# Optimization experiments

Hardware: AMD Instinct MI355X
Metric: run time of the kernel (lower is better)

Reference implementation:

```python
import jax, jax.numpy as jnp
import numpy as np

N_NODES = 100000
N_EDGES = 1600000
F_IN = 64
F_HID = 64


def setup_inputs() -> dict:
    key = jax.random.key(0)
    k = jax.random.split(key, 6)
    x = jax.random.normal(k[0], (N_NODES, F_IN), dtype=jnp.float32)
    edge_src = jax.random.randint(k[1], (N_EDGES,), 0, N_NODES, dtype=jnp.int32)
    edge_dst = jax.random.randint(k[2], (N_EDGES,), 0, N_NODES, dtype=jnp.int32)
    W1 = jax.random.normal(k[3], (2 * F_IN, F_HID), dtype=jnp.float32) * 0.05
    b1 = jnp.zeros((F_HID,), dtype=jnp.float32)
    W2 = jax.random.normal(k[4], (2 * F_HID, F_HID), dtype=jnp.float32) * 0.05
    b2 = jnp.zeros((F_HID,), dtype=jnp.float32)
    return {"x": x, "edge_src": edge_src, "edge_dst": edge_dst,
            "W1": W1, "b1": b1, "W2": W2, "b2": b2}


def _mean_aggregate(x, edge_src, edge_dst):
    # gather neighbor features along edges, segment-mean into destination nodes
    msgs = x[edge_src]                                            # [E, F]
    summed = jax.ops.segment_sum(msgs, edge_dst, num_segments=N_NODES)  # [N, F]
    cnt = jax.ops.segment_sum(jnp.ones_like(edge_dst, dtype=x.dtype),
                              edge_dst, num_segments=N_NODES)      # [N]
    # nodes with no neighbors -> zero vector (matches torch loop behavior)
    return summed / jnp.maximum(cnt, 1.0)[:, None]


def _sage_layer(x, edge_src, edge_dst, W, b):
    neigh_mean = _mean_aggregate(x, edge_src, edge_dst)
    h = jnp.concatenate([x, neigh_mean], axis=1)                  # [N, 2F]
    return jax.nn.relu(h @ W + b)


def reference(x, edge_src, edge_dst, W1, b1, W2, b2):
    h = _sage_layer(x, edge_src, edge_dst, W1, b1)
    h = _sage_layer(h, edge_src, edge_dst, W2, b2)
    return h
```

## Files before the change

kernel.cpp:

```cpp
#include <hip/hip_runtime.h>
#include <hip/hip_bf16.h>


constexpr int N_NODES = 100000;
constexpr int N_EDGES = 1600000;
constexpr int F = 64;
constexpr int SH = 9;
constexpr int SPAN = 1 << SH;
constexpr int NBK = 256;
constexpr int NBK_USED = (N_NODES + SPAN - 1) / SPAN;
constexpr int PART_T = 512;
constexpr int PART_E = 4096;
constexpr int PART_BLOCKS = (N_EDGES + PART_E - 1) / PART_E;
constexpr int COUNT_BLOCKS = (N_EDGES + 2047) / 2048;
constexpr int LDW = 136;

typedef short short8 __attribute__((ext_vector_type(8)));
typedef float floatx4 __attribute__((ext_vector_type(4)));

__device__ __forceinline__ float bf2f(ushort u) {
    union { unsigned int i; float f; } c; c.i = (unsigned int)u << 16; return c.f;
}
__device__ __forceinline__ ushort f2bf(float v) {
    union { float f; unsigned int i; } c; c.f = v;
    unsigned int r = c.i + 0x7fffu + ((c.i >> 16) & 1u);
    return (ushort)(r >> 16);
}


__global__ void __launch_bounds__(256)
count_kernel(const int* __restrict__ edst, int* __restrict__ bcnt) {
    __shared__ int lb[NBK];
    int t = threadIdx.x;
    lb[t] = 0;
    __syncthreads();
    int base = blockIdx.x * 2048;
    #pragma unroll
    for (int k = 0; k < 8; ++k) {
        int e = base + k * 256 + t;
        if (e < N_EDGES) atomicAdd(&lb[edst[e] >> SH], 1);
    }
    __syncthreads();
    if (lb[t]) atomicAdd(&bcnt[t], lb[t]);
}

__global__ void __launch_bounds__(512)
scan_prep_kernel(const int* __restrict__ bcnt, int* __restrict__ bbase,
                 int* __restrict__ bcur, int* __restrict__ rp,
                 const float* __restrict__ W1, const float* __restrict__ W2,
                 ushort* __restrict__ Wt1, ushort* __restrict__ Wt2) {
    __shared__ int sb[NBK];
    int t = threadIdx.x;
    if (t < NBK) sb[t] = bcnt[t];
    __syncthreads();
    if (t == 0) {
        int run = 0;
        for (int i = 0; i < NBK; ++i) { int v = sb[i]; sb[i] = run; run += v; }
        rp[N_NODES] = run;
    }
    __syncthreads();
    if (t < NBK) { bbase[t] = sb[t]; bcur[t] = sb[t]; }
    for (int i = t; i < 2 * F * F; i += 512) {
        int k = i >> 6, f = i & 63;
        Wt1[f * LDW + k] = f2bf(W1[i]);
        Wt2[f * LDW + k] = f2bf(W2[i]);
    }
}

__global__ void __launch_bounds__(PART_T)
part_kernel(const int* __restrict__ esrc, const int* __restrict__ edst,
            int* __restrict__ bcur, int2* __restrict__ ebuf) {
    __shared__ int cnt[NBK];
    __shared__ int lbase[NBK];
    __shared__ int gbase[NBK];
    __shared__ int2 stage[PART_E];
    int t = threadIdx.x;
    if (t < NBK) cnt[t] = 0;
    __syncthreads();
    int base = blockIdx.x * PART_E;
    int2 ed[8]; int bk[8]; int rk[8];
    #pragma unroll
    for (int k = 0; k < 8; ++k) {
        int e = base + k * PART_T + t;
        if (e < N_EDGES) {
            ed[k].x = esrc[e];
            ed[k].y = edst[e];
            bk[k] = ed[k].y >> SH;
            rk[k] = atomicAdd(&cnt[bk[k]], 1);
        } else {
            bk[k] = -1; rk[k] = 0; ed[k] = make_int2(0, 0);
        }
    }
    __syncthreads();
    {
        int v = 0;
        if (t < NBK) { v = cnt[t]; lbase[t] = v; }
        __syncthreads();
        for (int off = 1; off < NBK; off <<= 1) {
            int add = 0;
            if (t < NBK && t >= off) add = lbase[t - off];
            __syncthreads();
            if (t < NBK) lbase[t] += add;
            __syncthreads();
        }
        if (t < NBK) lbase[t] -= v;
    }
    __syncthreads();
    if (t < NBK) gbase[t] = cnt[t] ? atomicAdd(&bcur[t], cnt[t]) : 0;
    __syncthreads();
    #pragma unroll
    for (int k = 0; k < 8; ++k)
        if (bk[k] >= 0) stage[lbase[bk[k]] + rk[k]] = ed[k];
    __syncthreads();
    {
        int w = t >> 6, lane = t & 63;
        for (int b = w * 32; b < w * 32 + 32; ++b) {
            int len = cnt[b], l0 = lbase[b], g0 = gbase[b];
            for (int i = lane; i < len; i += 64) ebuf[g0 + i] = stage[l0 + i];
        }
    }
}

__global__ void __launch_bounds__(512)
csr_bucket_kernel(const int2* __restrict__ ebuf, const int* __restrict__ bbase,
                  const int* __restrict__ bcnt,
                  int* __restrict__ rp, int* __restrict__ ss) {
    __shared__ int sdeg[SPAN];
    __shared__ int sc[SPAN];
    int b = blockIdx.x;
    int lo = b << SH;
    int bstart = bbase[b];
    int bn = bcnt[b];
    int t = threadIdx.x;

    sdeg[t] = 0;
    __syncthreads();
    for (int i = t; i < bn; i += 512)
        atomicAdd(&sdeg[ebuf[bstart + i].y - lo], 1);
    __syncthreads();

    int a = sdeg[t];
    sc[t] = a;
    __syncthreads();
    for (int off = 1; off < SPAN; off <<= 1) {
        int v = sc[t];
        int add = (t >= off) ? sc[t - off] : 0;
        __syncthreads();
        sc[t] = v + add;
        __syncthreads();
    }
    int ex = sc[t] - a;
    sdeg[t] = ex;
    if (lo + t < N_NODES) rp[lo + t] = bstart + ex;
    __syncthreads();

    for (int i = t; i < bn; i += 512) {
        int2 p = ebuf[bstart + i];
        int pos = atomicAdd(&sdeg[p.y - lo], 1);
        ss[bstart + pos] = p.x;
    }
}

__global__ void __launch_bounds__(256)
conv_kernel(const float* __restrict__ x, ushort* __restrict__ xh) {
    int i = blockIdx.x * 256 + threadIdx.x;
    float4 v = ((const float4*)x)[i];
    ushort4 o;
    o.x = f2bf(v.x); o.y = f2bf(v.y); o.z = f2bf(v.z); o.w = f2bf(v.w);
    ((ushort4*)xh)[i] = o;
}

__global__ void __launch_bounds__(512)
fused_sage_kernel(const ushort* __restrict__ xh,
                  const int* __restrict__ rp,
                  const int* __restrict__ ss,
                  const ushort* __restrict__ Wt,
                  const float* __restrict__ bias,
                  ushort* __restrict__ out_bf,
                  float* __restrict__ out_f)
{
    __shared__ ushort sWt[F * LDW];
    __shared__ ushort cin[32 * LDW];

    {
        const int* src = (const int*)Wt;
        int* dst = (int*)sWt;
        for (int i = threadIdx.x; i < F * LDW / 2; i += 512) dst[i] = src[i];
    }

    const int w    = threadIdx.x >> 6;
    const int lane = threadIdx.x & 63;
    const int half = lane >> 5;
    const int p    = lane & 31;

    const unsigned int* __restrict__ xw = (const unsigned int*)xh;

    for (int q = 0; q < 4; ++q) {
        const int n = blockIdx.x * 32 + w * 4 + q;
        int start = rp[n];
        int end   = rp[n + 1];
        float ax = 0.0f, ay = 0.0f;

        int i = start;
        for (; i + 8 <= end; i += 8) {
            int e0 = i + half;
            int s0 = ss[e0], s1 = ss[e0 + 2], s2 = ss[e0 + 4], s3 = ss[e0 + 6];
            unsigned int u0 = xw[(size_t)s0 * 32 + p];
            unsigned int u1 = xw[(size_t)s1 * 32 + p];
            unsigned int u2 = xw[(size_t)s2 * 32 + p];
            unsigned int u3 = xw[(size_t)s3 * 32 + p];
            ax += bf2f((ushort)u0) + bf2f((ushort)u1)
                + bf2f((ushort)u2) + bf2f((ushort)u3);
            ay += bf2f((ushort)(u0 >> 16)) + bf2f((ushort)(u1 >> 16))
                + bf2f((ushort)(u2 >> 16)) + bf2f((ushort)(u3 >> 16));
        }
        for (; i + 2 <= end; i += 2) {
            int s0 = ss[i + half];
            unsigned int u0 = xw[(size_t)s0 * 32 + p];
            ax += bf2f((ushort)u0);
            ay += bf2f((ushort)(u0 >> 16));
        }
        if (i < end && half == 0) {
            int s0 = ss[i];
            unsigned int u0 = xw[(size_t)s0 * 32 + p];
            ax += bf2f((ushort)u0);
            ay += bf2f((ushort)(u0 >> 16));
        }
        ax += __shfl_xor(ax, 32);
        ay += __shfl_xor(ay, 32);

        if (half == 0) {
            unsigned int* crow = (unsigned int*)&cin[(w * 4 + q) * LDW];
            crow[p] = xw[(size_t)n * 32 + p];
            float scale = 1.0f / fmaxf((float)(end - start), 1.0f);
            unsigned int lo = f2bf(ax * scale);
            unsigned int hi = f2bf(ay * scale);
            crow[32 + p] = (hi << 16) | lo;
        }
    }
    __syncthreads();

    const int Mt = w >> 2, Nt = w & 3;
    const int r16 = lane & 15, g4 = lane >> 4;
    floatx4 acc = {0.0f, 0.0f, 0.0f, 0.0f};
    #pragma unroll
    for (int ks = 0; ks < 4; ++ks) {
        short8 a = *(const short8*)&cin[(Mt * 16 + r16) * LDW + ks * 32 + g4 * 8];
        short8 b = *(const short8*)&sWt[(Nt * 16 + r16) * LDW + ks * 32 + g4 * 8];
        acc = __builtin_amdgcn_mfma_f32_16x16x32_bf16(a, b, acc, 0, 0, 0);
    }
    const int feat = Nt * 16 + r16;
    const float bv = bias[feat];
    #pragma unroll
    for (int reg = 0; reg < 4; ++reg) {
        int node = blockIdx.x * 32 + Mt * 16 + g4 * 4 + reg;
        float r = fmaxf(acc[reg] + bv, 0.0f);
        if (out_bf) out_bf[(size_t)node * F + feat] = f2bf(r);
        if (out_f)  out_f [(size_t)node * F + feat] = r;
    }
}

extern "C" void kernel_launch(void* const* d_in, const int* in_sizes, int n_in,
                              void* d_out, int out_size, void* d_ws, size_t ws_size,
                              hipStream_t stream) {
    const float* x    = (const float*)d_in[0];
    const int*   esrc = (const int*)d_in[1];
    const int*   edst = (const int*)d_in[2];
    const float* W1   = (const float*)d_in[3];
    const float* b1   = (const float*)d_in[4];
    const float* W2   = (const float*)d_in[5];
    const float* b2   = (const float*)d_in[6];
    float* out = (float*)d_out;

    int*    bcnt   = (int*)d_ws;
    int*    bbase  = bcnt + NBK;
    int*    bcur   = bbase + NBK;
    int*    rp     = bcur + NBK;
    int*    ss     = rp + (N_NODES + 8);
    ushort* xh     = (ushort*)(ss + N_EDGES);
    ushort* h1h    = xh + (size_t)N_NODES * F;
    int2*   ebuf   = (int2*)h1h;
    ushort* Wt1g   = h1h + (size_t)N_NODES * F;
    ushort* Wt2g   = Wt1g + F * LDW;

    const int NB = N_NODES / 32;
    const int CB = (N_NODES * F / 4) / 256;

    hipMemsetAsync(bcnt, 0, NBK * 4, stream);
    count_kernel<<<COUNT_BLOCKS, 256, 0, stream>>>(edst, bcnt);
    scan_prep_kernel<<<1, 512, 0, stream>>>(bcnt, bbase, bcur, rp,
                                            W1, W2, Wt1g, Wt2g);
    part_kernel<<<PART_BLOCKS, PART_T, 0, stream>>>(esrc, edst, bcur, ebuf);
    csr_bucket_kernel<<<NBK_USED, 512, 0, stream>>>(ebuf, bbase, bcnt, rp, ss);
    conv_kernel<<<CB, 256, 0, stream>>>(x, xh);

    fused_sage_kernel<<<NB, 512, 0, stream>>>(xh,  rp, ss, Wt1g, b1, h1h, nullptr);
    fused_sage_kernel<<<NB, 512, 0, stream>>>(h1h, rp, ss, Wt2g, b2, nullptr, out);
}
```

Baseline: 303.5 us.

## Merge count and bf16 conversion kernels; assign one node per half-wave in aggregation

The edge-bucket count kernel and the fp32-to-bf16 feature conversion are merged into one launch, with blocks split by index range, which removes a kernel launch and lets the two independent jobs overlap. In the fused SAGE kernel each 32-lane half-wave now aggregates its own node over all of that node's edges, instead of two halves splitting one node's edges and combining them with a cross-lane shuffle. This removes the shuffle and the idle half during the store, and issues eight gathers per iteration per half. The cost is more divergence between the two halves when neighboring nodes have different degrees.

```diff
diff --git a/kernel.cpp b/kernel.cpp
--- a/kernel.cpp
+++ b/kernel.cpp
@@ -13,6 +13,7 @@
 constexpr int PART_E = 4096;
 constexpr int PART_BLOCKS = (N_EDGES + PART_E - 1) / PART_E;
 constexpr int COUNT_BLOCKS = (N_EDGES + 2047) / 2048;
+constexpr int CONV_BLOCKS = (N_NODES * F / 4) / 256;
 constexpr int LDW = 136;
 
 typedef short short8 __attribute__((ext_vector_type(8)));
@@ -27,21 +28,29 @@
     return (ushort)(r >> 16);
 }
 
-
 __global__ void __launch_bounds__(256)
-count_kernel(const int* __restrict__ edst, int* __restrict__ bcnt) {
-    __shared__ int lb[NBK];
-    int t = threadIdx.x;
-    lb[t] = 0;
-    __syncthreads();
-    int base = blockIdx.x * 2048;
-    #pragma unroll
-    for (int k = 0; k < 8; ++k) {
-        int e = base + k * 256 + t;
-        if (e < N_EDGES) atomicAdd(&lb[edst[e] >> SH], 1);
-    }
-    __syncthreads();
-    if (lb[t]) atomicAdd(&bcnt[t], lb[t]);
+count_conv_kernel(const int* __restrict__ edst, int* __restrict__ bcnt,
+                  const float* __restrict__ x, ushort* __restrict__ xh) {
+    int t = threadIdx.x;
+    if (blockIdx.x < COUNT_BLOCKS) {
+        __shared__ int lb[NBK];
+        lb[t] = 0;
+        __syncthreads();
+        int base = blockIdx.x * 2048;
+        #pragma unroll
+        for (int k = 0; k < 8; ++k) {
+            int e = base + k * 256 + t;
+            if (e < N_EDGES) atomicAdd(&lb[edst[e] >> SH], 1);
+        }
+        __syncthreads();
+        if (lb[t]) atomicAdd(&bcnt[t], lb[t]);
+    } else {
+        int i = (blockIdx.x - COUNT_BLOCKS) * 256 + t;
+        float4 v = ((const float4*)x)[i];
+        ushort4 o;
+        o.x = f2bf(v.x); o.y = f2bf(v.y); o.z = f2bf(v.z); o.w = f2bf(v.w);
+        ((ushort4*)xh)[i] = o;
+    }
 }
 
 __global__ void __launch_bounds__(512)
@@ -159,15 +168,6 @@
         int pos = atomicAdd(&sdeg[p.y - lo], 1);
         ss[bstart + pos] = p.x;
     }
-}
-
-__global__ void __launch_bounds__(256)
-conv_kernel(const float* __restrict__ x, ushort* __restrict__ xh) {
-    int i = blockIdx.x * 256 + threadIdx.x;
-    float4 v = ((const float4*)x)[i];
-    ushort4 o;
-    o.x = f2bf(v.x); o.y = f2bf(v.y); o.z = f2bf(v.z); o.w = f2bf(v.w);
-    ((ushort4*)xh)[i] = o;
 }
 
 __global__ void __launch_bounds__(512)
@@ -195,48 +195,47 @@
 
     const unsigned int* __restrict__ xw = (const unsigned int*)xh;
 
-    for (int q = 0; q < 4; ++q) {
-        const int n = blockIdx.x * 32 + w * 4 + q;
+    #pragma unroll
+    for (int q = 0; q < 2; ++q) {
+        const int n_row = w * 4 + half * 2 + q;
+        const int n = blockIdx.x * 32 + n_row;
         int start = rp[n];
         int end   = rp[n + 1];
         float ax = 0.0f, ay = 0.0f;
 
         int i = start;
         for (; i + 8 <= end; i += 8) {
-            int e0 = i + half;
-            int s0 = ss[e0], s1 = ss[e0 + 2], s2 = ss[e0 + 4], s3 = ss[e0 + 6];
+            int s0 = ss[i],     s1 = ss[i + 1], s2 = ss[i + 2], s3 = ss[i + 3];
+            int s4 = ss[i + 4], s5 = ss[i + 5], s6 = ss[i + 6], s7 = ss[i + 7];
             unsigned int u0 = xw[(size_t)s0 * 32 + p];
             unsigned int u1 = xw[(size_t)s1 * 32 + p];
             unsigned int u2 = xw[(size_t)s2 * 32 + p];
             unsigned int u3 = xw[(size_t)s3 * 32 + p];
+            unsigned int u4 = xw[(size_t)s4 * 32 + p];
+            unsigned int u5 = xw[(size_t)s5 * 32 + p];
+            unsigned int u6 = xw[(size_t)s6 * 32 + p];
+            unsigned int u7 = xw[(size_t)s7 * 32 + p];
             ax += bf2f((ushort)u0) + bf2f((ushort)u1)
-                + bf2f((ushort)u2) + bf2f((ushort)u3);
+                + bf2f((ushort)u2) + bf2f((ushort)u3)
+                + bf2f((ushort)u4) + bf2f((ushort)u5)
+                + bf2f((ushort)u6) + bf2f((ushort)u7);
             ay += bf2f((ushort)(u0 >> 16)) + bf2f((ushort)(u1 >> 16))
-                + bf2f((ushort)(u2 >> 16)) + bf2f((ushort)(u3 >> 16));
-        }
-        for (; i + 2 <= end; i += 2) {
-            int s0 = ss[i + half];
-            unsigned int u0 = xw[(size_t)s0 * 32 + p];
+                + bf2f((ushort)(u2 >> 16)) + bf2f((ushort)(u3 >> 16))
+                + bf2f((ushort)(u4 >> 16)) + bf2f((ushort)(u5 >> 16))
+                + bf2f((ushort)(u6 >> 16)) + bf2f((ushort)(u7 >> 16));
+        }
+        for (; i < end; ++i) {
+            unsigned int u0 = xw[(size_t)ss[i] * 32 + p];
             ax += bf2f((ushort)u0);
             ay += bf2f((ushort)(u0 >> 16));
         }
-        if (i < end && half == 0) {
-            int s0 = ss[i];
-            unsigned int u0 = xw[(size_t)s0 * 32 + p];
-            ax += bf2f((ushort)u0);
-            ay += bf2f((ushort)(u0 >> 16));
-        }
-        ax += __shfl_xor(ax, 32);
-        ay += __shfl_xor(ay, 32);
-
-        if (half == 0) {
-            unsigned int* crow = (unsigned int*)&cin[(w * 4 + q) * LDW];
-            crow[p] = xw[(size_t)n * 32 + p];
-            float scale = 1.0f / fmaxf((float)(end - start), 1.0f);
-            unsigned int lo = f2bf(ax * scale);
-            unsigned int hi = f2bf(ay * scale);
-            crow[32 + p] = (hi << 16) | lo;
-        }
+
+        unsigned int* crow = (unsigned int*)&cin[n_row * LDW];
+        crow[p] = xw[(size_t)n * 32 + p];
+        float scale = 1.0f / fmaxf((float)(end - start), 1.0f);
+        unsigned int lo = f2bf(ax * scale);
+        unsigned int hi = f2bf(ay * scale);
+        crow[32 + p] = (hi << 16) | lo;
     }
     __syncthreads();
 
@@ -284,15 +283,14 @@
     ushort* Wt2g   = Wt1g + F * LDW;
 
     const int NB = N_NODES / 32;
-    const int CB = (N_NODES * F / 4) / 256;
 
     hipMemsetAsync(bcnt, 0, NBK * 4, stream);
-    count_kernel<<<COUNT_BLOCKS, 256, 0, stream>>>(edst, bcnt);
+    count_conv_kernel<<<COUNT_BLOCKS + CONV_BLOCKS, 256, 0, stream>>>(
+        edst, bcnt, x, xh);
     scan_prep_kernel<<<1, 512, 0, stream>>>(bcnt, bbase, bcur, rp,
                                             W1, W2, Wt1g, Wt2g);
     part_kernel<<<PART_BLOCKS, PART_T, 0, stream>>>(esrc, edst, bcur, ebuf);
     csr_bucket_kernel<<<NBK_USED, 512, 0, stream>>>(ebuf, bbase, bcnt, rp, ss);
-    conv_kernel<<<CB, 256, 0, stream>>>(x, xh);
 
     fused_sage_kernel<<<NB, 512, 0, stream>>>(xh,  rp, ss, Wt1g, b1, h1h, nullptr);
     fused_sage_kernel<<<NB, 512, 0, stream>>>(h1h, rp, ss, Wt2g, b2, nullptr, out);
```

Result: faster. 294.7 us (-2.9%).
